# Performance work log

Hardware: AMD Instinct MI355X
Metric: run time of the kernel (lower is better)

Reference implementation:

```python
import jax, jax.numpy as jnp
import numpy as np

N_NODES = 100000
N_EDGES = 1600000
IN_DIM = 128
HIDDEN = 128
OUT_DIM = 64


def setup_inputs() -> dict:
    key = jax.random.key(0)
    ks = jax.random.split(key, 10)
    s = 0.05
    return {
        "x": jax.random.normal(ks[0], (N_NODES, IN_DIM), jnp.float32),
        "edge_index": jax.random.randint(ks[1], (2, N_EDGES), 0, N_NODES, dtype=jnp.int64),
        "w_l0": jax.random.normal(ks[2], (IN_DIM, HIDDEN), jnp.float32) * s,
        "b_l0": jnp.zeros((HIDDEN,), jnp.float32),
        "w_r0": jax.random.normal(ks[3], (IN_DIM, HIDDEN), jnp.float32) * s,
        "w_l1": jax.random.normal(ks[4], (HIDDEN, HIDDEN), jnp.float32) * s,
        "b_l1": jnp.zeros((HIDDEN,), jnp.float32),
        "w_r1": jax.random.normal(ks[5], (HIDDEN, HIDDEN), jnp.float32) * s,
        "w_out": jax.random.normal(ks[6], (HIDDEN, OUT_DIM), jnp.float32) * s,
        "b_out": jnp.zeros((OUT_DIM,), jnp.float32),
    }


def _sage_conv(x, src, dst, w_l, b_l, w_r, num_nodes):
    # mean-aggregate source features at destination nodes (PyG SAGEConv, aggr='mean')
    msgs = x[src]                                             # [E, D] gather
    agg = jax.ops.segment_sum(msgs, dst, num_segments=num_nodes)
    deg = jax.ops.segment_sum(jnp.ones((src.shape[0],), x.dtype), dst,
                              num_segments=num_nodes)
    agg = agg / jnp.maximum(deg, 1.0)[:, None]                # isolated nodes -> 0
    return agg @ w_l + b_l + x @ w_r


def reference(x, edge_index, w_l0, b_l0, w_r0, w_l1, b_l1, w_r1, w_out, b_out):
    src, dst = edge_index[0], edge_index[1]
    n = x.shape[0]
    h = jax.nn.relu(_sage_conv(x, src, dst, w_l0, b_l0, w_r0, n))
    h = jax.nn.relu(_sage_conv(h, src, dst, w_l1, b_l1, w_r1, n))
    return jax.nn.sigmoid(h @ w_out + b_out)
```

## Files before the change

### kernel.cpp

```cpp
#include <hip/hip_runtime.h>
#include <hip/hip_bf16.h>
#include <cstdint>

#define N_NODES 100000
#define N_EDGES 1600000
#define DIM 128
#define K2 256
#define ODIM 64
#define NPB 64
#define CB 98
#define NREP 8
#define CAP1 2560
#define EPB 4096
#define NWAVE 16

typedef __hip_bfloat16 bf16;
typedef __attribute__((ext_vector_type(8))) short bfrag;
typedef __attribute__((ext_vector_type(4))) float f32x4;
typedef __attribute__((ext_vector_type(2))) float f32x2;

__device__ __forceinline__ void gload16(const void* g, void* l) {
  __builtin_amdgcn_global_load_lds((const __attribute__((address_space(1))) void*)g,
                                   (__attribute__((address_space(3))) void*)l, 16, 0, 0);
}

__global__ __launch_bounds__(1024) void k_bucket(const int* __restrict__ src,
                                                 const int* __restrict__ dst,
                                                 int* __restrict__ gcur,
                                                 uint32_t* __restrict__ bdata) {
  __shared__ int wh[NWAVE][CB];
  __shared__ int wcur[NWAVE][CB];
  __shared__ int hist[CB], hbase[CB], gstart[CB];
  __shared__ uint32_t ent[EPB];
  __shared__ uint8_t kslot[EPB];
  const int tid = threadIdx.x;
  const int wave = tid >> 6;
  const int rep = blockIdx.x & (NREP - 1);
  const int e0 = blockIdx.x * EPB;
  const int cnt = min(EPB, N_EDGES - e0);

  for (int i = tid; i < NWAVE * CB; i += 1024) {
    ((int*)wh)[i] = 0;
    ((int*)wcur)[i] = 0;
  }
  __syncthreads();

  const int me0 = e0 + tid * 4;
  int ss[4], dd[4];
  int nmine = max(0, min(4, N_EDGES - me0));
  if (nmine == 4) {
    *(int4*)ss = *(const int4*)(src + me0);
    *(int4*)dd = *(const int4*)(dst + me0);
  } else {
    for (int q = 0; q < nmine; ++q) { ss[q] = src[me0 + q]; dd[q] = dst[me0 + q]; }
  }

#pragma unroll
  for (int q = 0; q < 4; ++q)
    if (q < nmine) atomicAdd(&wh[wave][dd[q] >> 10], 1);
  __syncthreads();

  if (tid < CB) {
    int run = 0;
#pragma unroll
    for (int w = 0; w < NWAVE; ++w) {
      int c = wh[w][tid];
      wh[w][tid] = run;
      run += c;
    }
    hist[tid] = run;
  }
  __syncthreads();

  if (tid == 0) {
    int run = 0;
    for (int b = 0; b < CB; ++b) { hbase[b] = run; run += hist[b]; }
  }
  __syncthreads();

#pragma unroll
  for (int q = 0; q < 4; ++q)
    if (q < nmine) {
      int key = dd[q] >> 10;
      int r = atomicAdd(&wcur[wave][key], 1);
      int p = hbase[key] + wh[wave][key] + r;
      ent[p] = ((uint32_t)ss[q] << 10) | (uint32_t)(dd[q] & 1023);
      kslot[p] = (uint8_t)key;
    }
  __syncthreads();

  if (tid < CB && hist[tid] > 0)
    gstart[tid] = atomicAdd(&gcur[rep * CB + tid], hist[tid]);
  __syncthreads();

  for (int i = tid; i < cnt; i += 1024) {
    int k = kslot[i];
    int pos = gstart[k] + (i - hbase[k]);
    if (pos < CAP1)
      bdata[((size_t)(rep * CB + k)) * CAP1 + pos] = ent[i];
  }
}

__global__ __launch_bounds__(256) void k_csr(const uint32_t* __restrict__ bdata,
                                             const int* __restrict__ gcur,
                                             int* __restrict__ rowptr,
                                             int* __restrict__ col) {
  __shared__ int nc[1024], noff[1024];
  __shared__ int red[256];
  __shared__ int sz[NREP];
  const int b = blockIdx.x, tid = threadIdx.x;

  if (tid < NREP) sz[tid] = min(gcur[tid * CB + b], CAP1);

  int part = 0;
  for (int i = tid; i < NREP * b; i += 256) {
    int bp = i >> 3, r = i & 7;
    part += min(gcur[r * CB + bp], CAP1);
  }
  red[tid] = part;
  __syncthreads();
  for (int off = 128; off > 0; off >>= 1) {
    if (tid < off) red[tid] += red[tid + off];
    __syncthreads();
  }
  const int base = red[0];
  __syncthreads();

  for (int i = tid; i < 1024; i += 256) nc[i] = 0;
  __syncthreads();

  for (int r = 0; r < NREP; ++r) {
    int c = sz[r];
    const uint32_t* seg = bdata + ((size_t)(r * CB + b)) * CAP1;
    for (int i = tid; i < c; i += 256)
      atomicAdd(&nc[seg[i] & 1023], 1);
  }
  __syncthreads();

  int loc[4], s = 0;
#pragma unroll
  for (int q = 0; q < 4; ++q) { loc[q] = nc[tid * 4 + q]; s += loc[q]; }
  red[tid] = s;
  __syncthreads();
  for (int off = 1; off < 256; off <<= 1) {
    int add = (tid >= off) ? red[tid - off] : 0;
    __syncthreads();
    red[tid] += add;
    __syncthreads();
  }
  int p = red[tid] - s;
#pragma unroll
  for (int q = 0; q < 4; ++q) { noff[tid * 4 + q] = p; p += loc[q]; }
  __syncthreads();

  for (int i = tid; i < 1024; i += 256) {
    int n = b * 1024 + i;
    if (n < N_NODES) rowptr[n] = base + noff[i];
  }
  if (b == 0 && tid == 0) rowptr[N_NODES] = N_EDGES;

  for (int i = tid; i < 1024; i += 256) nc[i] = 0;
  __syncthreads();

  for (int r = 0; r < NREP; ++r) {
    int c = sz[r];
    const uint32_t* seg = bdata + ((size_t)(r * CB + b)) * CAP1;
    for (int i = tid; i < c; i += 256) {
      uint32_t e = seg[i];
      int n = e & 1023;
      int pos = atomicAdd(&nc[n], 1);
      col[base + noff[n] + pos] = (int)((e >> 10) << 7);
    }
  }
}

__global__ __launch_bounds__(256) void k_cvt(const float* __restrict__ x,
                                             bf16* __restrict__ xb,
                                             uint8_t* __restrict__ x8) {
  int i = (blockIdx.x * 256 + threadIdx.x) * 4;
  if (i >= N_NODES * DIM) return;
  float4 v = *(const float4*)(x + i);
  bf16 t[4];
  t[0] = __float2bfloat16(v.x);
  t[1] = __float2bfloat16(v.y);
  t[2] = __float2bfloat16(v.z);
  t[3] = __float2bfloat16(v.w);
  *(uint2*)(xb + i) = *(uint2*)t;
  int p8 = __builtin_amdgcn_cvt_pk_fp8_f32(v.x, v.y, 0, false);
  p8 = __builtin_amdgcn_cvt_pk_fp8_f32(v.z, v.w, p8, true);
  *(int*)(x8 + i) = p8;
}

__global__ __launch_bounds__(256) void k_prepw(const float* __restrict__ wl0,
                                               const float* __restrict__ wr0,
                                               const float* __restrict__ wl1,
                                               const float* __restrict__ wr1,
                                               const float* __restrict__ wo,
                                               bf16* __restrict__ WT0,
                                               bf16* __restrict__ WT1,
                                               bf16* __restrict__ WoT) {
  int g = blockIdx.x * 256 + threadIdx.x;
  if (g < 32768) {
    int j = g >> 8, k = g & 255;
    float v = (k < DIM) ? wl0[k * DIM + j] : wr0[(k - DIM) * DIM + j];
    WT0[g] = __float2bfloat16(v);
  } else if (g < 65536) {
    int gg = g - 32768;
    int j = gg >> 8, k = gg & 255;
    float v = (k < DIM) ? wl1[k * DIM + j] : wr1[(k - DIM) * DIM + j];
    WT1[gg] = __float2bfloat16(v);
  } else if (g < 65536 + 8192) {
    int gg = g - 65536;
    int j = gg >> 7, k = gg & 127;
    WoT[gg] = __float2bfloat16(wo[k * ODIM + j]);
  }
}

__device__ __forceinline__ void accv8(f32x2* acc, uint2 v) {
  f32x2 t0 = __builtin_amdgcn_cvt_pk_f32_fp8(v.x, false);
  f32x2 t1 = __builtin_amdgcn_cvt_pk_f32_fp8(v.x, true);
  f32x2 t2 = __builtin_amdgcn_cvt_pk_f32_fp8(v.y, false);
  f32x2 t3 = __builtin_amdgcn_cvt_pk_f32_fp8(v.y, true);
  acc[0] += t0; acc[1] += t1; acc[2] += t2; acc[3] += t3;
}

__global__ __launch_bounds__(256) void k_agg(const uint8_t* __restrict__ feat8,
                                             const int* __restrict__ rowptr,
                                             const int* __restrict__ colb,
                                             bf16* __restrict__ agg) {
  int gid = blockIdx.x * 256 + threadIdx.x;
  int node = gid >> 6;
  if (node >= N_NODES) return;
  int lane = gid & 63;
  int g = lane >> 4, lg = lane & 15;
  int beg = rowptr[node], end = rowptr[node + 1];
  const char* fb = (const char*)feat8 + lg * 8;

  f32x2 acc[4];
#pragma unroll
  for (int q = 0; q < 4; ++q) acc[q] = (f32x2){0.f, 0.f};

  int j = beg;
  for (; j + 16 <= end; j += 16) {
    int o0 = colb[j + g];
    int o1 = colb[j + 4 + g];
    int o2 = colb[j + 8 + g];
    int o3 = colb[j + 12 + g];
    uint2 v0 = *(const uint2*)(fb + o0);
    uint2 v1 = *(const uint2*)(fb + o1);
    uint2 v2 = *(const uint2*)(fb + o2);
    uint2 v3 = *(const uint2*)(fb + o3);
    accv8(acc, v0); accv8(acc, v1); accv8(acc, v2); accv8(acc, v3);
  }
  for (; j + 4 <= end; j += 4) {
    int o = colb[j + g];
    uint2 v = *(const uint2*)(fb + o);
    accv8(acc, v);
  }
  int rem = end - j;
  if (g < rem) {
    int o = colb[j + g];
    uint2 v = *(const uint2*)(fb + o);
    accv8(acc, v);
  }

#pragma unroll
  for (int q = 0; q < 4; ++q) {
#pragma unroll
    for (int c = 0; c < 2; ++c) {
      acc[q][c] += __shfl_xor(acc[q][c], 16, 64);
      acc[q][c] += __shfl_xor(acc[q][c], 32, 64);
    }
  }

  if (g == 0) {
    float inv = (end > beg) ? 1.0f / (float)(end - beg) : 0.f;
    union { uint32_t u[4]; uint4 v; } o;
#pragma unroll
    for (int q = 0; q < 4; ++q) {
      __hip_bfloat162 h;
      h.x = __float2bfloat16(acc[q][0] * inv);
      h.y = __float2bfloat16(acc[q][1] * inv);
      o.u[q] = *(uint32_t*)&h;
    }
    *(uint4*)(agg + (size_t)node * DIM + lg * 8) = o.v;
  }
}

__global__ __launch_bounds__(256) void k_sage(const bf16* __restrict__ agg,
                                              const bf16* __restrict__ xb,
                                              const bf16* __restrict__ WT,
                                              const float* __restrict__ bias,
                                              bf16* __restrict__ hout,
                                              uint8_t* __restrict__ h8) {
  __shared__ char sA[NPB * 512];
  const int tid = threadIdx.x;
  const int base = blockIdx.x * NPB;

#pragma unroll
  for (int i = 0; i < 8; ++i) {
    int c = tid + 256 * i;
    int row = c >> 5;
    int n = min(base + row, N_NODES - 1);
    int kcg = (c & 31) ^ (row & 7);
    const bf16* sp = (kcg < 16) ? (agg + (size_t)n * DIM + kcg * 8)
                                : (xb + (size_t)n * DIM + (kcg - 16) * 8);
    gload16(sp, sA + c * 16);
  }
  __syncthreads();

  const int w = tid >> 6, lane = tid & 63;
  const int j0 = w * 32;
  const int lrow = lane & 15, lk = lane >> 4;

  f32x4 acc[4][2];
#pragma unroll
  for (int mi = 0; mi < 4; ++mi)
#pragma unroll
    for (int ni = 0; ni < 2; ++ni)
      acc[mi][ni] = (f32x4){0.f, 0.f, 0.f, 0.f};

  for (int kt = 0; kt < 8; ++kt) {
    bfrag b0 = *(const bfrag*)(WT + (size_t)(j0 + lrow) * K2 + kt * 32 + lk * 8);
    bfrag b1 = *(const bfrag*)(WT + (size_t)(j0 + 16 + lrow) * K2 + kt * 32 + lk * 8);
#pragma unroll
    for (int mi = 0; mi < 4; ++mi) {
      int row = mi * 16 + lrow;
      int byte = (row * 512 + kt * 64 + lk * 16) ^ ((row & 7) << 4);
      bfrag a = *(const bfrag*)(sA + byte);
      acc[mi][0] = __builtin_amdgcn_mfma_f32_16x16x32_bf16(a, b0, acc[mi][0], 0, 0, 0);
      acc[mi][1] = __builtin_amdgcn_mfma_f32_16x16x32_bf16(a, b1, acc[mi][1], 0, 0, 0);
    }
  }

#pragma unroll
  for (int ni = 0; ni < 2; ++ni) {
    int colj = j0 + ni * 16 + lrow;
    float bv = bias[colj];
#pragma unroll
    for (int mi = 0; mi < 4; ++mi) {
#pragma unroll
      for (int r = 0; r < 4; ++r) {
        int n = base + mi * 16 + lk * 4 + r;
        if (n < N_NODES) {
          float v = fmaxf(acc[mi][ni][r] + bv, 0.f);
          hout[(size_t)n * DIM + colj] = __float2bfloat16(v);
          h8[(size_t)n * DIM + colj] =
              (uint8_t)(__builtin_amdgcn_cvt_pk_fp8_f32(v, v, 0, false) & 0xFF);
        }
      }
    }
  }
}

__global__ __launch_bounds__(256) void k_out(const bf16* __restrict__ agg,
                                             const bf16* __restrict__ xb,
                                             const bf16* __restrict__ WT,
                                             const float* __restrict__ bias,
                                             const bf16* __restrict__ WoT,
                                             const float* __restrict__ bo,
                                             float* __restrict__ out) {
  __shared__ char sA[NPB * 512];
  const int tid = threadIdx.x;
  const int base = blockIdx.x * NPB;

#pragma unroll
  for (int i = 0; i < 8; ++i) {
    int c = tid + 256 * i;
    int row = c >> 5;
    int n = min(base + row, N_NODES - 1);
    int kcg = (c & 31) ^ (row & 7);
    const bf16* sp = (kcg < 16) ? (agg + (size_t)n * DIM + kcg * 8)
                                : (xb + (size_t)n * DIM + (kcg - 16) * 8);
    gload16(sp, sA + c * 16);
  }
  __syncthreads();

  const int w = tid >> 6, lane = tid & 63;
  const int j0 = w * 32;
  const int lrow = lane & 15, lk = lane >> 4;

  f32x4 acc[4][2];
#pragma unroll
  for (int mi = 0; mi < 4; ++mi)
#pragma unroll
    for (int ni = 0; ni < 2; ++ni)
      acc[mi][ni] = (f32x4){0.f, 0.f, 0.f, 0.f};

  for (int kt = 0; kt < 8; ++kt) {
    bfrag b0 = *(const bfrag*)(WT + (size_t)(j0 + lrow) * K2 + kt * 32 + lk * 8);
    bfrag b1 = *(const bfrag*)(WT + (size_t)(j0 + 16 + lrow) * K2 + kt * 32 + lk * 8);
#pragma unroll
    for (int mi = 0; mi < 4; ++mi) {
      int row = mi * 16 + lrow;
      int byte = (row * 512 + kt * 64 + lk * 16) ^ ((row & 7) << 4);
      bfrag a = *(const bfrag*)(sA + byte);
      acc[mi][0] = __builtin_amdgcn_mfma_f32_16x16x32_bf16(a, b0, acc[mi][0], 0, 0, 0);
      acc[mi][1] = __builtin_amdgcn_mfma_f32_16x16x32_bf16(a, b1, acc[mi][1], 0, 0, 0);
    }
  }

  __syncthreads();
#pragma unroll
  for (int ni = 0; ni < 2; ++ni) {
    int colj = j0 + ni * 16 + lrow;
    float bv = bias[colj];
#pragma unroll
    for (int mi = 0; mi < 4; ++mi) {
#pragma unroll
      for (int r = 0; r < 4; ++r) {
        int row = mi * 16 + lk * 4 + r;
        float v = fmaxf(acc[mi][ni][r] + bv, 0.f);
        int byte = (row * 256 + colj * 2) ^ ((row & 7) << 4);
        *(bf16*)(sA + byte) = __float2bfloat16(v);
      }
    }
  }
  __syncthreads();

  const int jo = w * 16;
  f32x4 acc2[4];
#pragma unroll
  for (int mi = 0; mi < 4; ++mi) acc2[mi] = (f32x4){0.f, 0.f, 0.f, 0.f};

#pragma unroll
  for (int kt = 0; kt < 4; ++kt) {
    bfrag b = *(const bfrag*)(WoT + (size_t)(jo + lrow) * DIM + kt * 32 + lk * 8);
#pragma unroll
    for (int mi = 0; mi < 4; ++mi) {
      int row = mi * 16 + lrow;
      int byte = (row * 256 + kt * 64 + lk * 16) ^ ((row & 7) << 4);
      bfrag a = *(const bfrag*)(sA + byte);
      acc2[mi] = __builtin_amdgcn_mfma_f32_16x16x32_bf16(a, b, acc2[mi], 0, 0, 0);
    }
  }

  int colj = jo + lrow;
  float bv = bo[colj];
#pragma unroll
  for (int mi = 0; mi < 4; ++mi) {
#pragma unroll
    for (int r = 0; r < 4; ++r) {
      int n = base + mi * 16 + lk * 4 + r;
      if (n < N_NODES)
        out[(size_t)n * ODIM + colj] = 1.f / (1.f + __expf(-(acc2[mi][r] + bv)));
    }
  }
}

extern "C" void kernel_launch(void* const* d_in, const int* in_sizes, int n_in,
                              void* d_out, int out_size, void* d_ws, size_t ws_size,
                              hipStream_t stream) {
  const float* x     = (const float*)d_in[0];
  const int*   ei    = (const int*)d_in[1];
  const float* w_l0  = (const float*)d_in[2];
  const float* b_l0  = (const float*)d_in[3];
  const float* w_r0  = (const float*)d_in[4];
  const float* w_l1  = (const float*)d_in[5];
  const float* b_l1  = (const float*)d_in[6];
  const float* w_r1  = (const float*)d_in[7];
  const float* w_out = (const float*)d_in[8];
  const float* b_out = (const float*)d_in[9];
  float* out = (float*)d_out;

  const int* src = ei;
  const int* dst = ei + N_EDGES;

  char* ws = (char*)d_ws;
  int*      rowptr = (int*)(ws);
  int*      gcur   = (int*)(ws + (512u << 10));
  int*      col    = (int*)(ws + (1u << 20));
  uint32_t* bdata  = (uint32_t*)(ws + (8u << 20));
  uint8_t*  x8     = (uint8_t*)(ws + (8u << 20));
  uint8_t*  h08    = (uint8_t*)(ws + (8u << 20));
  bf16*     WT0    = (bf16*)(ws + (21u << 20));
  bf16*     WT1    = (bf16*)(ws + (21u << 20) + 65536);
  bf16*     WoT    = (bf16*)(ws + (21u << 20) + 131072);
  bf16*     aggb   = (bf16*)(ws + (22ull << 20));
  bf16*     h0b    = (bf16*)(ws + (48ull << 20));
  bf16*     xb     = (bf16*)(ws + (74ull << 20));

  hipMemsetAsync(gcur, 0, NREP * CB * sizeof(int), stream);
  k_bucket<<<(N_EDGES + EPB - 1) / EPB, 1024, 0, stream>>>(src, dst, gcur, bdata);
  k_csr   <<<CB, 256, 0, stream>>>(bdata, gcur, rowptr, col);

  k_cvt  <<<(N_NODES * DIM / 4 + 255) / 256, 256, 0, stream>>>(x, xb, x8);
  k_prepw<<<(65536 + 8192 + 255) / 256, 256, 0, stream>>>(w_l0, w_r0, w_l1, w_r1, w_out,
                                                          WT0, WT1, WoT);

  const int ablocks = (N_NODES * 64 + 255) / 256;
  const int gblocks = (N_NODES + NPB - 1) / NPB;

  k_agg <<<ablocks, 256, 0, stream>>>(x8, rowptr, col, aggb);
  k_sage<<<gblocks, 256, 0, stream>>>(aggb, xb, WT0, b_l0, h0b, h08);

  k_agg<<<ablocks, 256, 0, stream>>>(h08, rowptr, col, aggb);
  k_out<<<gblocks, 256, 0, stream>>>(aggb, h0b, WT1, b_l1, WoT, b_out, out);
}
```

Before: 233.2 us.

## Double GEMM node tile to 128 with 512 threads, widen cvt, nontemporal stores

The node tile per block in the SAGE and output GEMM kernels doubles from 64 to 128 rows, with 512 threads split into 4 column groups × 2 row groups, so each weight fragment load serves more rows and fewer blocks are launched. The conversion kernel now handles 8 floats per thread with 16-byte bf16 stores. Aggregation and hidden-layer outputs are written with nontemporal stores to limit cache pollution. The larger tile uses 64KB of shared memory per block, which may reduce occupancy, and nontemporal writes could hurt the next kernel, which reads those buffers straight back.

Measured after the change: 271.0 us. 1.16x slower.

```diff
diff --git a/kernel.cpp b/kernel.cpp
--- a/kernel.cpp
+++ b/kernel.cpp
@@ -7,7 +7,7 @@
 #define DIM 128
 #define K2 256
 #define ODIM 64
-#define NPB 64
+#define NPB 128
 #define CB 98
 #define NREP 8
 #define CAP1 2560
@@ -18,6 +18,7 @@
 typedef __attribute__((ext_vector_type(8))) short bfrag;
 typedef __attribute__((ext_vector_type(4))) float f32x4;
 typedef __attribute__((ext_vector_type(2))) float f32x2;
+typedef __attribute__((ext_vector_type(4))) unsigned int u32x4;
 
 __device__ __forceinline__ void gload16(const void* g, void* l) {
   __builtin_amdgcn_global_load_lds((const __attribute__((address_space(1))) void*)g,
@@ -177,18 +178,22 @@
 __global__ __launch_bounds__(256) void k_cvt(const float* __restrict__ x,
                                              bf16* __restrict__ xb,
                                              uint8_t* __restrict__ x8) {
-  int i = (blockIdx.x * 256 + threadIdx.x) * 4;
+  int i = (blockIdx.x * 256 + threadIdx.x) * 8;
   if (i >= N_NODES * DIM) return;
-  float4 v = *(const float4*)(x + i);
-  bf16 t[4];
-  t[0] = __float2bfloat16(v.x);
-  t[1] = __float2bfloat16(v.y);
-  t[2] = __float2bfloat16(v.z);
-  t[3] = __float2bfloat16(v.w);
-  *(uint2*)(xb + i) = *(uint2*)t;
-  int p8 = __builtin_amdgcn_cvt_pk_fp8_f32(v.x, v.y, 0, false);
-  p8 = __builtin_amdgcn_cvt_pk_fp8_f32(v.z, v.w, p8, true);
-  *(int*)(x8 + i) = p8;
+  float4 v0 = *(const float4*)(x + i);
+  float4 v1 = *(const float4*)(x + i + 4);
+  bf16 t[8];
+  t[0] = __float2bfloat16(v0.x); t[1] = __float2bfloat16(v0.y);
+  t[2] = __float2bfloat16(v0.z); t[3] = __float2bfloat16(v0.w);
+  t[4] = __float2bfloat16(v1.x); t[5] = __float2bfloat16(v1.y);
+  t[6] = __float2bfloat16(v1.z); t[7] = __float2bfloat16(v1.w);
+  *(uint4*)(xb + i) = *(uint4*)t;
+  int lo = __builtin_amdgcn_cvt_pk_fp8_f32(v0.x, v0.y, 0, false);
+  lo = __builtin_amdgcn_cvt_pk_fp8_f32(v0.z, v0.w, lo, true);
+  int hi = __builtin_amdgcn_cvt_pk_fp8_f32(v1.x, v1.y, 0, false);
+  hi = __builtin_amdgcn_cvt_pk_fp8_f32(v1.z, v1.w, hi, true);
+  uint2 o; o.x = (uint32_t)lo; o.y = (uint32_t)hi;
+  *(uint2*)(x8 + i) = o;
 }
 
 __global__ __launch_bounds__(256) void k_prepw(const float* __restrict__ wl0,
@@ -275,19 +280,19 @@
 
   if (g == 0) {
     float inv = (end > beg) ? 1.0f / (float)(end - beg) : 0.f;
-    union { uint32_t u[4]; uint4 v; } o;
+    u32x4 o;
 #pragma unroll
     for (int q = 0; q < 4; ++q) {
       __hip_bfloat162 h;
       h.x = __float2bfloat16(acc[q][0] * inv);
       h.y = __float2bfloat16(acc[q][1] * inv);
-      o.u[q] = *(uint32_t*)&h;
-    }
-    *(uint4*)(agg + (size_t)node * DIM + lg * 8) = o.v;
-  }
-}
-
-__global__ __launch_bounds__(256) void k_sage(const bf16* __restrict__ agg,
+      o[q] = *(uint32_t*)&h;
+    }
+    __builtin_nontemporal_store(o, (u32x4*)(agg + (size_t)node * DIM + lg * 8));
+  }
+}
+
+__global__ __launch_bounds__(512) void k_sage(const bf16* __restrict__ agg,
                                               const bf16* __restrict__ xb,
                                               const bf16* __restrict__ WT,
                                               const float* __restrict__ bias,
@@ -299,7 +304,7 @@
 
 #pragma unroll
   for (int i = 0; i < 8; ++i) {
-    int c = tid + 256 * i;
+    int c = tid + 512 * i;
     int row = c >> 5;
     int n = min(base + row, N_NODES - 1);
     int kcg = (c & 31) ^ (row & 7);
@@ -310,7 +315,8 @@
   __syncthreads();
 
   const int w = tid >> 6, lane = tid & 63;
-  const int j0 = w * 32;
+  const int j0 = (w & 3) * 32;
+  const int r0 = (w >> 2) * 64;
   const int lrow = lane & 15, lk = lane >> 4;
 
   f32x4 acc[4][2];
@@ -325,7 +331,7 @@
     bfrag b1 = *(const bfrag*)(WT + (size_t)(j0 + 16 + lrow) * K2 + kt * 32 + lk * 8);
 #pragma unroll
     for (int mi = 0; mi < 4; ++mi) {
-      int row = mi * 16 + lrow;
+      int row = r0 + mi * 16 + lrow;
       int byte = (row * 512 + kt * 64 + lk * 16) ^ ((row & 7) << 4);
       bfrag a = *(const bfrag*)(sA + byte);
       acc[mi][0] = __builtin_amdgcn_mfma_f32_16x16x32_bf16(a, b0, acc[mi][0], 0, 0, 0);
@@ -341,19 +347,21 @@
     for (int mi = 0; mi < 4; ++mi) {
 #pragma unroll
       for (int r = 0; r < 4; ++r) {
-        int n = base + mi * 16 + lk * 4 + r;
+        int n = base + r0 + mi * 16 + lk * 4 + r;
         if (n < N_NODES) {
           float v = fmaxf(acc[mi][ni][r] + bv, 0.f);
-          hout[(size_t)n * DIM + colj] = __float2bfloat16(v);
-          h8[(size_t)n * DIM + colj] =
-              (uint8_t)(__builtin_amdgcn_cvt_pk_fp8_f32(v, v, 0, false) & 0xFF);
+          union { bf16 h; uint16_t u; } cv;
+          cv.h = __float2bfloat16(v);
+          __builtin_nontemporal_store(cv.u, (uint16_t*)&hout[(size_t)n * DIM + colj]);
+          uint8_t f8 = (uint8_t)(__builtin_amdgcn_cvt_pk_fp8_f32(v, v, 0, false) & 0xFF);
+          __builtin_nontemporal_store(f8, &h8[(size_t)n * DIM + colj]);
         }
       }
     }
   }
 }
 
-__global__ __launch_bounds__(256) void k_out(const bf16* __restrict__ agg,
+__global__ __launch_bounds__(512) void k_out(const bf16* __restrict__ agg,
                                              const bf16* __restrict__ xb,
                                              const bf16* __restrict__ WT,
                                              const float* __restrict__ bias,
@@ -366,7 +374,7 @@
 
 #pragma unroll
   for (int i = 0; i < 8; ++i) {
-    int c = tid + 256 * i;
+    int c = tid + 512 * i;
     int row = c >> 5;
     int n = min(base + row, N_NODES - 1);
     int kcg = (c & 31) ^ (row & 7);
@@ -377,7 +385,8 @@
   __syncthreads();
 
   const int w = tid >> 6, lane = tid & 63;
-  const int j0 = w * 32;
+  const int j0 = (w & 3) * 32;
+  const int r0 = (w >> 2) * 64;
   const int lrow = lane & 15, lk = lane >> 4;
 
   f32x4 acc[4][2];
@@ -392,7 +401,7 @@
     bfrag b1 = *(const bfrag*)(WT + (size_t)(j0 + 16 + lrow) * K2 + kt * 32 + lk * 8);
 #pragma unroll
     for (int mi = 0; mi < 4; ++mi) {
-      int row = mi * 16 + lrow;
+      int row = r0 + mi * 16 + lrow;
       int byte = (row * 512 + kt * 64 + lk * 16) ^ ((row & 7) << 4);
       bfrag a = *(const bfrag*)(sA + byte);
       acc[mi][0] = __builtin_amdgcn_mfma_f32_16x16x32_bf16(a, b0, acc[mi][0], 0, 0, 0);
@@ -409,7 +418,7 @@
     for (int mi = 0; mi < 4; ++mi) {
 #pragma unroll
       for (int r = 0; r < 4; ++r) {
-        int row = mi * 16 + lk * 4 + r;
+        int row = r0 + mi * 16 + lk * 4 + r;
         float v = fmaxf(acc[mi][ni][r] + bv, 0.f);
         int byte = (row * 256 + colj * 2) ^ ((row & 7) << 4);
         *(bf16*)(sA + byte) = __float2bfloat16(v);
@@ -418,7 +427,8 @@
   }
   __syncthreads();
 
-  const int jo = w * 16;
+  const int jo = (w & 3) * 16;
+  const int r2 = (w >> 2) * 64;
   f32x4 acc2[4];
 #pragma unroll
   for (int mi = 0; mi < 4; ++mi) acc2[mi] = (f32x4){0.f, 0.f, 0.f, 0.f};
@@ -428,7 +438,7 @@
     bfrag b = *(const bfrag*)(WoT + (size_t)(jo + lrow) * DIM + kt * 32 + lk * 8);
 #pragma unroll
     for (int mi = 0; mi < 4; ++mi) {
-      int row = mi * 16 + lrow;
+      int row = r2 + mi * 16 + lrow;
       int byte = (row * 256 + kt * 64 + lk * 16) ^ ((row & 7) << 4);
       bfrag a = *(const bfrag*)(sA + byte);
       acc2[mi] = __builtin_amdgcn_mfma_f32_16x16x32_bf16(a, b, acc2[mi], 0, 0, 0);
@@ -441,7 +451,7 @@
   for (int mi = 0; mi < 4; ++mi) {
 #pragma unroll
     for (int r = 0; r < 4; ++r) {
-      int n = base + mi * 16 + lk * 4 + r;
+      int n = base + r2 + mi * 16 + lk * 4 + r;
       if (n < N_NODES)
         out[(size_t)n * ODIM + colj] = 1.f / (1.f + __expf(-(acc2[mi][r] + bv)));
     }
@@ -484,7 +494,7 @@
   k_bucket<<<(N_EDGES + EPB - 1) / EPB, 1024, 0, stream>>>(src, dst, gcur, bdata);
   k_csr   <<<CB, 256, 0, stream>>>(bdata, gcur, rowptr, col);
 
-  k_cvt  <<<(N_NODES * DIM / 4 + 255) / 256, 256, 0, stream>>>(x, xb, x8);
+  k_cvt  <<<(N_NODES * DIM / 8 + 255) / 256, 256, 0, stream>>>(x, xb, x8);
   k_prepw<<<(65536 + 8192 + 255) / 256, 256, 0, stream>>>(w_l0, w_r0, w_l1, w_r1, w_out,
                                                           WT0, WT1, WoT);
 
@@ -492,8 +502,8 @@
   const int gblocks = (N_NODES + NPB - 1) / NPB;
 
   k_agg <<<ablocks, 256, 0, stream>>>(x8, rowptr, col, aggb);
-  k_sage<<<gblocks, 256, 0, stream>>>(aggb, xb, WT0, b_l0, h0b, h08);
+  k_sage<<<gblocks, 512, 0, stream>>>(aggb, xb, WT0, b_l0, h0b, h08);
 
   k_agg<<<ablocks, 256, 0, stream>>>(h08, rowptr, col, aggb);
-  k_out<<<gblocks, 256, 0, stream>>>(aggb, h0b, WT1, b_l1, WoT, b_out, out);
-}
+  k_out<<<gblocks, 512, 0, stream>>>(aggb, h0b, WT1, b_l1, WoT, b_out, out);
+}
```
